# Kernel optimization log

Hardware: AMD Instinct MI355X
Metric: run time of the kernel (lower is better)

The kernel has to match this reference:

```python
import jax, jax.numpy as jnp
import numpy as np

K = 3          # deformable conv kernel size
PAD = 1        # (K-1)//2
G = 4          # deformable groups


def setup_inputs() -> dict:
    key = jax.random.key(0)
    k1, k2, k3, k4 = jax.random.split(key, 4)
    B, Cin, Cout, H, W = 8, 256, 256, 64, 64
    NA = 9  # num_anchors
    x = jax.random.normal(k1, (B, Cin, H, W), jnp.float32)
    shape = jax.random.normal(k2, (B, NA * 4, H, W), jnp.float32)
    # conv_offset: 1x1 conv, no bias -> weight (G*2*K*K, NA*4); std=0.1 per init_weights
    w_off = jax.random.normal(k3, (G * 2 * K * K, NA * 4), jnp.float32) * 0.1
    # conv_adaption (DeformConv, no bias): weight (Cout, Cin, K, K); std=0.01
    w_def = jax.random.normal(k4, (Cout, Cin, K, K), jnp.float32) * 0.01
    return {"x": x, "shape": shape, "w_off": w_off, "w_def": w_def}


def _deform_conv(x, offset, w):
    """DCNv1: x (B,Cin,H,W), offset (B,G*2*K*K,H,W) interleaved (dy,dx) per tap, w (Cout,Cin,K,K)."""
    B, Cin, H, W = x.shape
    Cout = w.shape[0]
    K2 = K * K
    Cg = Cin // G
    off = offset.reshape(B, G, K2, 2, H, W)  # [..., 0]=dy, [..., 1]=dx (mmcv layout)
    ky, kx = jnp.meshgrid(jnp.arange(K) - PAD, jnp.arange(K) - PAD, indexing='ij')
    ky = ky.reshape(K2).astype(x.dtype)
    kx = kx.reshape(K2).astype(x.dtype)
    hh = jnp.arange(H, dtype=x.dtype)
    ww = jnp.arange(W, dtype=x.dtype)
    # sampling positions: p = p0 + kernel_tap + learned_offset  -> (B,G,K2,H,W)
    py = off[:, :, :, 0] + ky[None, None, :, None, None] + hh[None, None, None, :, None]
    px = off[:, :, :, 1] + kx[None, None, :, None, None] + ww[None, None, None, None, :]

    y0f = jnp.floor(py)
    x0f = jnp.floor(px)
    wy1 = py - y0f
    wx1 = px - x0f
    y0 = y0f.astype(jnp.int32)
    x0 = x0f.astype(jnp.int32)

    img = x.reshape(B, G, Cg, H, W).transpose(0, 1, 3, 4, 2)  # (B,G,H,W,Cg) channels-last for gather
    b_idx = jnp.arange(B)[:, None, None, None, None]
    g_idx = jnp.arange(G)[None, :, None, None, None]

    def gather(yi, xi):
        valid = (yi >= 0) & (yi < H) & (xi >= 0) & (xi < W)
        yc = jnp.clip(yi, 0, H - 1)
        xc = jnp.clip(xi, 0, W - 1)
        v = img[b_idx, g_idx, yc, xc]  # (B,G,K2,H,W,Cg)
        return v * valid[..., None].astype(v.dtype)

    val = (gather(y0, x0) * ((1 - wy1) * (1 - wx1))[..., None]
           + gather(y0, x0 + 1) * ((1 - wy1) * wx1)[..., None]
           + gather(y0 + 1, x0) * (wy1 * (1 - wx1))[..., None]
           + gather(y0 + 1, x0 + 1) * (wy1 * wx1)[..., None])  # (B,G,K2,H,W,Cg)

    wr = w.reshape(Cout, G, Cg, K2)
    return jnp.einsum('bgkhwc,ogck->bohw', val, wr)


def reference(x, shape, w_off, w_def):
    # conv_offset: 1x1 conv, no bias, on detached shape prediction
    offset = jnp.einsum('bihw,oi->bohw', jax.lax.stop_gradient(shape), w_off)
    return jax.nn.relu(_deform_conv(x, offset, w_def))
```

## Files before the change

### kernel.cpp

```cpp
#include <hip/hip_runtime.h>
#include <hip/hip_bf16.h>


#define NPIX 32768
#define NGK  36
#define HW   4096
#define WSTRIDE 16384

typedef __attribute__((ext_vector_type(8))) short short8;
typedef __attribute__((ext_vector_type(4))) float f32x4;
typedef unsigned short u16;
typedef unsigned int u32;

__device__ __forceinline__ float bfu_lo(u32 u) {
    union { u32 u; float f; } cv; cv.u = u << 16; return cv.f;
}
__device__ __forceinline__ float bfu_hi(u32 u) {
    union { u32 u; float f; } cv; cv.u = u & 0xFFFF0000u; return cv.f;
}
__device__ __forceinline__ u16 f2bf(float f) {
    union { float f; u32 u; } cv;
    cv.f = f;
    u32 u = cv.u + 0x7FFFu + ((cv.u >> 16) & 1u);
    return (u16)(u >> 16);
}

__global__ __launch_bounds__(256) void kprep(const float* __restrict__ x,
                                             const float* __restrict__ shape,
                                             const float* __restrict__ w_off,
                                             const float* __restrict__ w_def,
                                             float2* __restrict__ pos,
                                             u16* __restrict__ xT,
                                             u16* __restrict__ wF) {
    __shared__ __align__(16) float smem[64 * 65];
    int tid = threadIdx.x;
    int blk = blockIdx.x;

    if (blk < 128) {
        float* wo = smem;
        for (int i = tid; i < 72 * 36; i += 256) wo[i] = w_off[i];
        __syncthreads();
        int pix = blk * 256 + tid;
        int b = pix >> 12, hw = pix & 4095;
        int h = hw >> 6, w = hw & 63;
        float s[36];
#pragma unroll
        for (int i = 0; i < 36; ++i) s[i] = shape[((b * 36 + i) << 12) + hw];
        for (int gk = 0; gk < 36; ++gk) {
            float oy = 0.f, ox = 0.f;
            const float* wy = &wo[(gk * 2 + 0) * 36];
            const float* wx = &wo[(gk * 2 + 1) * 36];
#pragma unroll
            for (int i = 0; i < 36; ++i) { oy += s[i] * wy[i]; ox += s[i] * wx[i]; }
            int k = gk % 9;
            pos[gk * NPIX + pix] = make_float2(oy + (float)(k / 3 - 1) + (float)h,
                                               ox + (float)(k % 3 - 1) + (float)w);
        }
    } else if (blk < 2176) {
        float (*tile)[65] = (float (*)[65])smem;
        int xb  = blk - 128;
        int bg  = xb >> 6;
        int hw0 = (xb & 63) << 6;
        int hwo = tid & 63;
#pragma unroll
        for (int i = 0; i < 16; ++i) {
            int c = (tid >> 6) + (i << 2);
            tile[c][hwo] = x[((bg << 6) + c) * HW + hw0 + hwo];
        }
        __syncthreads();
        int hw = tid >> 2;
        int cb4 = (tid & 3) << 4;
        short8 r0, r1;
#pragma unroll
        for (int j = 0; j < 8; ++j) {
            r0[j] = (short)f2bf(tile[cb4 + j][hw]);
            r1[j] = (short)f2bf(tile[cb4 + 8 + j][hw]);
        }
        u16* dst = xT + (((bg << 12) + hw0 + hw) << 6) + cb4;
        *(short8*)dst = r0;
        *(short8*)(dst + 8) = r1;
    } else {
        int idx = (blk - 2176) * 256 + tid;
        int c = idx & 63;
        int o = (idx >> 6) & 255;
        int gk = idx >> 14;
        int g = gk / 9, k = gk - g * 9;
        float v = w_def[((o << 8) + (g << 6) + c) * 9 + k];
        int wid = o >> 5, of = (o >> 4) & 1, olo = o & 15;
        int kc = c >> 5, cgran = (c >> 3) & 3, j = c & 7;
        int lane = (cgran << 4) | olo;
        wF[(gk << 14) + (wid << 11) + (of << 10) + (kc << 9) + (lane << 3) + j] = f2bf(v);
    }
}

struct Samp {
    short8 v00, v01, v10, v11;
    float w00, w01, w10, w11;
    int dst;
};

__device__ __forceinline__ Samp sample_issue_rec(uint2 ra, float4 rw,
                                                 const u16* __restrict__ slab,
                                                 int sp, int sck) {
    Samp s;
    int a00 = ra.x & 0xFFFF, a01 = ra.x >> 16;
    int a10 = ra.y & 0xFFFF, a11 = ra.y >> 16;
    const u16* base = slab + (sck << 3);
    s.v00 = *(const short8*)(base + (a00 << 6));
    s.v01 = *(const short8*)(base + (a01 << 6));
    s.v10 = *(const short8*)(base + (a10 << 6));
    s.v11 = *(const short8*)(base + (a11 << 6));
    s.w00 = rw.x; s.w01 = rw.y; s.w10 = rw.z; s.w11 = rw.w;
    s.dst = (sp << 6) + ((sck ^ (sp & 7)) << 3);
    return s;
}

__device__ __forceinline__ void sample_finish(const Samp& s, u16* __restrict__ sVb) {
    union { short8 s8; u32 u[4]; } A, Bc, C, D;
    A.s8 = s.v00; Bc.s8 = s.v01; C.s8 = s.v10; D.s8 = s.v11;
    union { u32 u[4]; short8 s8; } R;
#pragma unroll
    for (int j = 0; j < 4; ++j) {
        float lo0 = fmaf(s.w00, bfu_lo(A.u[j]), s.w01 * bfu_lo(Bc.u[j]));
        float lo1 = fmaf(s.w10, bfu_lo(C.u[j]), s.w11 * bfu_lo(D.u[j]));
        float hi0 = fmaf(s.w00, bfu_hi(A.u[j]), s.w01 * bfu_hi(Bc.u[j]));
        float hi1 = fmaf(s.w10, bfu_hi(C.u[j]), s.w11 * bfu_hi(D.u[j]));
        __hip_bfloat162 pk = __float22bfloat162_rn(make_float2(lo0 + lo1, hi0 + hi1));
        union { __hip_bfloat162 b; u32 u; } cv; cv.b = pk;
        R.u[j] = cv.u;
    }
    *(short8*)(sVb + s.dst) = R.s8;
}

__device__ __forceinline__ void mfma_phase(const short8 wcur[4], const u16* __restrict__ Vb,
                                           int lane, f32x4 acc[2][4]) {
    __builtin_amdgcn_s_setprio(1);
#pragma unroll
    for (int kc = 0; kc < 2; ++kc) {
        int cs = ((kc << 5) + ((lane >> 4) << 3)) ^ ((lane & 7) << 3);
        short8 bfr[4];
#pragma unroll
        for (int pf = 0; pf < 4; ++pf)
            bfr[pf] = *(const short8*)(Vb + (((pf << 4) + (lane & 15)) << 6) + cs);
#pragma unroll
        for (int of = 0; of < 2; ++of)
#pragma unroll
            for (int pf = 0; pf < 4; ++pf)
                acc[of][pf] = __builtin_amdgcn_mfma_f32_16x16x32_bf16(
                    wcur[of * 2 + kc], bfr[pf], acc[of][pf], 0, 0, 0);
    }
    __builtin_amdgcn_s_setprio(0);
}

__global__ __launch_bounds__(512, 4) void kmain(
    const u16* __restrict__ xT,
    const float2* __restrict__ pos,
    const u16* __restrict__ wF, float* __restrict__ out)
{
    __shared__ __align__(16) u16 sV[2][64 * 64];
    __shared__ __align__(16) uint2 sRA[NGK * 64];
    __shared__ __align__(16) float4 sRW[NGK * 64];

    int tid = threadIdx.x;
    int pixbase = blockIdx.x << 6;
    int b = pixbase >> 12;

    int sp = tid >> 3, sck = tid & 7;
    int lane = tid & 63, wid = tid >> 6;
    int o0 = wid << 5;

    const u16* slabB = xT + ((size_t)b << 20);
    const u16* wlbase = wF + (wid << 11) + (lane << 3);

    f32x4 acc[2][4];
#pragma unroll
    for (int i = 0; i < 2; ++i)
#pragma unroll
        for (int j = 0; j < 4; ++j)
            acc[i][j] = (f32x4){0.f, 0.f, 0.f, 0.f};

    short8 wC[4], wN[4];
    Samp s;

    for (int i = tid; i < NGK * 64; i += 512) {
        int gk = i >> 6, px = i & 63;
        float2 p = pos[gk * NPIX + pixbase + px];
        float py = p.x, pxx = p.y;
        float y0f = floorf(py), x0f = floorf(pxx);
        float fy = py - y0f, fx = pxx - x0f;
        int y0 = (int)y0f, x0 = (int)x0f;
        int y1 = y0 + 1, x1 = x0 + 1;
        float vy0 = (y0 >= 0 && y0 < 64) ? 1.f : 0.f;
        float vy1 = (y1 >= 0 && y1 < 64) ? 1.f : 0.f;
        float vx0 = (x0 >= 0 && x0 < 64) ? 1.f : 0.f;
        float vx1 = (x1 >= 0 && x1 < 64) ? 1.f : 0.f;
        float w00 = (1.f - fy) * (1.f - fx) * vy0 * vx0;
        float w01 = (1.f - fy) * fx * vy0 * vx1;
        float w10 = fy * (1.f - fx) * vy1 * vx0;
        float w11 = fy * fx * vy1 * vx1;
        int yc0 = min(max(y0, 0), 63), yc1 = min(max(y1, 0), 63);
        int xc0 = min(max(x0, 0), 63), xc1 = min(max(x1, 0), 63);
        u32 A = (u32)((yc0 << 6) | xc0) | ((u32)((yc0 << 6) | xc1) << 16);
        u32 Bp = (u32)((yc1 << 6) | xc0) | ((u32)((yc1 << 6) | xc1) << 16);
        sRA[i] = make_uint2(A, Bp);
        sRW[i] = make_float4(w00, w01, w10, w11);
    }

    wC[0] = *(const short8*)(wlbase);
    wC[1] = *(const short8*)(wlbase + 512);
    wC[2] = *(const short8*)(wlbase + 1024);
    wC[3] = *(const short8*)(wlbase + 1536);
    __syncthreads();

    {
        Samp s0 = sample_issue_rec(sRA[sp], sRW[sp], slabB, sp, sck);
        sample_finish(s0, sV[0]);
    }
    __syncthreads();

#define TAP_BODY(T, WCUR, WNXT)                                                  \
    {                                                                            \
        const int t_ = (T);                                                      \
        const u16* wn = wlbase + (t_ + 1) * WSTRIDE;                             \
        WNXT[0] = *(const short8*)(wn);                                          \
        WNXT[1] = *(const short8*)(wn + 512);                                    \
        WNXT[2] = *(const short8*)(wn + 1024);                                   \
        WNXT[3] = *(const short8*)(wn + 1536);                                   \
        s = sample_issue_rec(sRA[((t_ + 1) << 6) + sp], sRW[((t_ + 1) << 6) + sp], \
                             slabB + (((t_ + 1) / 9) << 18), sp, sck);           \
        __builtin_amdgcn_sched_barrier(0);                                       \
        mfma_phase(WCUR, sV[t_ & 1], lane, acc);                                 \
        sample_finish(s, sV[(t_ & 1) ^ 1]);                                      \
        __syncthreads();                                                         \
    }

    for (int t = 0; t < 34; t += 2) {
        TAP_BODY(t,     wC, wN)
        TAP_BODY(t + 1, wN, wC)
    }
#undef TAP_BODY

    {
        const u16* wn = wlbase + 35 * WSTRIDE;
        wN[0] = *(const short8*)(wn);
        wN[1] = *(const short8*)(wn + 512);
        wN[2] = *(const short8*)(wn + 1024);
        wN[3] = *(const short8*)(wn + 1536);
        s = sample_issue_rec(sRA[(35 << 6) + sp], sRW[(35 << 6) + sp],
                             slabB + (3 << 18), sp, sck);
        __builtin_amdgcn_sched_barrier(0);
        mfma_phase(wC, sV[0], lane, acc);
        sample_finish(s, sV[1]);
        __syncthreads();
    }
    mfma_phase(wN, sV[1], lane, acc);

    int hwb = pixbase & 4095;
    int obase = (b << 8) + o0 + ((lane >> 4) << 2);
#pragma unroll
    for (int of = 0; of < 2; ++of) {
#pragma unroll
        for (int pf = 0; pf < 4; ++pf) {
            float* op = out + ((obase + (of << 4)) << 12) + hwb + (pf << 4) + (lane & 15);
#pragma unroll
            for (int r = 0; r < 4; ++r)
                op[r << 12] = fmaxf(acc[of][pf][r], 0.f);
        }
    }
}

extern "C" void kernel_launch(void* const* d_in, const int* in_sizes, int n_in,
                              void* d_out, int out_size, void* d_ws, size_t ws_size,
                              hipStream_t stream) {
    const float* x     = (const float*)d_in[0];
    const float* shape = (const float*)d_in[1];
    const float* w_off = (const float*)d_in[2];
    const float* w_def = (const float*)d_in[3];
    float* out = (float*)d_out;

    float2* pos = (float2*)d_ws;
    u16*    wF  = (u16*)(pos + NGK * NPIX);
    u16*    xT  = wF + NGK * 256 * 64;

    kprep<<<4480, 256, 0, stream>>>(x, shape, w_off, w_def, pos, xT, wF);
    kmain<<<NPIX / 64, 512, 0, stream>>>(xT, pos, wF, out);
}
```

Before: 86.06 us.

## Process two taps per barrier with four LDS buffers and compact sample records

Restructures the main loop so each iteration samples two taps ahead into a four-slot LDS ring and runs two MFMA phases per barrier, halving the number of __syncthreads. The per-pixel bilinear weights are no longer stored as float4; validity flags are packed into the spare bits of the address record and only the fractional parts are stored, with the weights rebuilt at sample time. This cuts LDS record traffic and barrier count, at the cost of more registers held in flight (two sample sets plus two weight fragments) and some extra ALU work per sample, which may lower occupancy.

```diff
diff --git a/kernel.cpp b/kernel.cpp
--- a/kernel.cpp
+++ b/kernel.cpp
@@ -99,18 +99,25 @@
     int dst;
 };
 
-__device__ __forceinline__ Samp sample_issue_rec(uint2 ra, float4 rw,
+__device__ __forceinline__ Samp sample_issue_rec(uint2 ra, float2 fxy,
                                                  const u16* __restrict__ slab,
                                                  int sp, int sck) {
     Samp s;
-    int a00 = ra.x & 0xFFFF, a01 = ra.x >> 16;
-    int a10 = ra.y & 0xFFFF, a11 = ra.y >> 16;
+    u32 rx = ra.x, ry = ra.y;
+    int a00 = rx & 0xFFF, a01 = (rx >> 16) & 0xFFF;
+    int a10 = ry & 0xFFF, a11 = (ry >> 16) & 0xFFF;
     const u16* base = slab + (sck << 3);
     s.v00 = *(const short8*)(base + (a00 << 6));
     s.v01 = *(const short8*)(base + (a01 << 6));
     s.v10 = *(const short8*)(base + (a10 << 6));
     s.v11 = *(const short8*)(base + (a11 << 6));
-    s.w00 = rw.x; s.w01 = rw.y; s.w10 = rw.z; s.w11 = rw.w;
+    float fy = fxy.x, fx = fxy.y;
+    float wy0 = (rx & 0x1000u) ? (1.f - fy) : 0.f;
+    float wy1 = (rx & 0x2000u) ? fy : 0.f;
+    float wx0 = (rx & 0x4000u) ? (1.f - fx) : 0.f;
+    float wx1 = (rx & 0x8000u) ? fx : 0.f;
+    s.w00 = wy0 * wx0; s.w01 = wy0 * wx1;
+    s.w10 = wy1 * wx0; s.w11 = wy1 * wx1;
     s.dst = (sp << 6) + ((sck ^ (sp & 7)) << 3);
     return s;
 }
@@ -157,9 +164,9 @@
     const float2* __restrict__ pos,
     const u16* __restrict__ wF, float* __restrict__ out)
 {
-    __shared__ __align__(16) u16 sV[2][64 * 64];
+    __shared__ __align__(16) u16 sV[4][4096];
     __shared__ __align__(16) uint2 sRA[NGK * 64];
-    __shared__ __align__(16) float4 sRW[NGK * 64];
+    __shared__ __align__(16) float2 sFX[NGK * 64];
 
     int tid = threadIdx.x;
     int pixbase = blockIdx.x << 6;
@@ -179,81 +186,85 @@
         for (int j = 0; j < 4; ++j)
             acc[i][j] = (f32x4){0.f, 0.f, 0.f, 0.f};
 
-    short8 wC[4], wN[4];
-    Samp s;
+    short8 wE[4], wO[4];
 
     for (int i = tid; i < NGK * 64; i += 512) {
         int gk = i >> 6, px = i & 63;
         float2 p = pos[gk * NPIX + pixbase + px];
-        float py = p.x, pxx = p.y;
-        float y0f = floorf(py), x0f = floorf(pxx);
-        float fy = py - y0f, fx = pxx - x0f;
+        float y0f = floorf(p.x), x0f = floorf(p.y);
+        float fy = p.x - y0f, fx = p.y - x0f;
         int y0 = (int)y0f, x0 = (int)x0f;
         int y1 = y0 + 1, x1 = x0 + 1;
-        float vy0 = (y0 >= 0 && y0 < 64) ? 1.f : 0.f;
-        float vy1 = (y1 >= 0 && y1 < 64) ? 1.f : 0.f;
-        float vx0 = (x0 >= 0 && x0 < 64) ? 1.f : 0.f;
-        float vx1 = (x1 >= 0 && x1 < 64) ? 1.f : 0.f;
-        float w00 = (1.f - fy) * (1.f - fx) * vy0 * vx0;
-        float w01 = (1.f - fy) * fx * vy0 * vx1;
-        float w10 = fy * (1.f - fx) * vy1 * vx0;
-        float w11 = fy * fx * vy1 * vx1;
+        u32 flags = 0;
+        if (y0 >= 0 && y0 < 64) flags |= 0x1000u;
+        if (y1 >= 0 && y1 < 64) flags |= 0x2000u;
+        if (x0 >= 0 && x0 < 64) flags |= 0x4000u;
+        if (x1 >= 0 && x1 < 64) flags |= 0x8000u;
         int yc0 = min(max(y0, 0), 63), yc1 = min(max(y1, 0), 63);
         int xc0 = min(max(x0, 0), 63), xc1 = min(max(x1, 0), 63);
-        u32 A = (u32)((yc0 << 6) | xc0) | ((u32)((yc0 << 6) | xc1) << 16);
-        u32 Bp = (u32)((yc1 << 6) | xc0) | ((u32)((yc1 << 6) | xc1) << 16);
-        sRA[i] = make_uint2(A, Bp);
-        sRW[i] = make_float4(w00, w01, w10, w11);
-    }
-
-    wC[0] = *(const short8*)(wlbase);
-    wC[1] = *(const short8*)(wlbase + 512);
-    wC[2] = *(const short8*)(wlbase + 1024);
-    wC[3] = *(const short8*)(wlbase + 1536);
+        u32 a00 = (u32)((yc0 << 6) | xc0), a01 = (u32)((yc0 << 6) | xc1);
+        u32 a10 = (u32)((yc1 << 6) | xc0), a11 = (u32)((yc1 << 6) | xc1);
+        sRA[i] = make_uint2(a00 | flags | (a01 << 16), a10 | (a11 << 16));
+        sFX[i] = make_float2(fy, fx);
+    }
+
+    wE[0] = *(const short8*)(wlbase);
+    wE[1] = *(const short8*)(wlbase + 512);
+    wE[2] = *(const short8*)(wlbase + 1024);
+    wE[3] = *(const short8*)(wlbase + 1536);
     __syncthreads();
 
     {
-        Samp s0 = sample_issue_rec(sRA[sp], sRW[sp], slabB, sp, sck);
+        Samp s0 = sample_issue_rec(sRA[sp], sFX[sp], slabB, sp, sck);
         sample_finish(s0, sV[0]);
+        Samp s1 = sample_issue_rec(sRA[64 + sp], sFX[64 + sp], slabB, sp, sck);
+        sample_finish(s1, sV[1]);
     }
     __syncthreads();
 
-#define TAP_BODY(T, WCUR, WNXT)                                                  \
-    {                                                                            \
-        const int t_ = (T);                                                      \
-        const u16* wn = wlbase + (t_ + 1) * WSTRIDE;                             \
-        WNXT[0] = *(const short8*)(wn);                                          \
-        WNXT[1] = *(const short8*)(wn + 512);                                    \
-        WNXT[2] = *(const short8*)(wn + 1024);                                   \
-        WNXT[3] = *(const short8*)(wn + 1536);                                   \
-        s = sample_issue_rec(sRA[((t_ + 1) << 6) + sp], sRW[((t_ + 1) << 6) + sp], \
-                             slabB + (((t_ + 1) / 9) << 18), sp, sck);           \
-        __builtin_amdgcn_sched_barrier(0);                                       \
-        mfma_phase(WCUR, sV[t_ & 1], lane, acc);                                 \
-        sample_finish(s, sV[(t_ & 1) ^ 1]);                                      \
-        __syncthreads();                                                         \
-    }
-
-    for (int t = 0; t < 34; t += 2) {
-        TAP_BODY(t,     wC, wN)
-        TAP_BODY(t + 1, wN, wC)
-    }
-#undef TAP_BODY
+    for (int p = 0; p < 17; ++p) {
+        int t0 = p << 1;
+        int cur = (p & 1) << 1, nxt = cur ^ 2;
+
+        const u16* wop = wlbase + (t0 + 1) * WSTRIDE;
+        wO[0] = *(const short8*)(wop);
+        wO[1] = *(const short8*)(wop + 512);
+        wO[2] = *(const short8*)(wop + 1024);
+        wO[3] = *(const short8*)(wop + 1536);
+
+        int ta = t0 + 2, tb = t0 + 3;
+        Samp sA = sample_issue_rec(sRA[(ta << 6) + sp], sFX[(ta << 6) + sp],
+                                   slabB + ((ta / 9) << 18), sp, sck);
+        Samp sB = sample_issue_rec(sRA[(tb << 6) + sp], sFX[(tb << 6) + sp],
+                                   slabB + ((tb / 9) << 18), sp, sck);
+        __builtin_amdgcn_sched_barrier(0);
+
+        mfma_phase(wE, &sV[cur][0], lane, acc);
+
+        const u16* wep = wlbase + (t0 + 2) * WSTRIDE;
+        wE[0] = *(const short8*)(wep);
+        wE[1] = *(const short8*)(wep + 512);
+        wE[2] = *(const short8*)(wep + 1024);
+        wE[3] = *(const short8*)(wep + 1536);
+        __builtin_amdgcn_sched_barrier(0);
+
+        mfma_phase(wO, &sV[cur + 1][0], lane, acc);
+
+        sample_finish(sA, &sV[nxt][0]);
+        sample_finish(sB, &sV[nxt + 1][0]);
+        __syncthreads();
+    }
 
     {
-        const u16* wn = wlbase + 35 * WSTRIDE;
-        wN[0] = *(const short8*)(wn);
-        wN[1] = *(const short8*)(wn + 512);
-        wN[2] = *(const short8*)(wn + 1024);
-        wN[3] = *(const short8*)(wn + 1536);
-        s = sample_issue_rec(sRA[(35 << 6) + sp], sRW[(35 << 6) + sp],
-                             slabB + (3 << 18), sp, sck);
+        const u16* wop = wlbase + 35 * WSTRIDE;
+        wO[0] = *(const short8*)(wop);
+        wO[1] = *(const short8*)(wop + 512);
+        wO[2] = *(const short8*)(wop + 1024);
+        wO[3] = *(const short8*)(wop + 1536);
         __builtin_amdgcn_sched_barrier(0);
-        mfma_phase(wC, sV[0], lane, acc);
-        sample_finish(s, sV[1]);
-        __syncthreads();
-    }
-    mfma_phase(wN, sV[1], lane, acc);
+        mfma_phase(wE, &sV[2][0], lane, acc);
+        mfma_phase(wO, &sV[3][0], lane, acc);
+    }
 
     int hwb = pixbase & 4095;
     int obase = (b << 8) + o0 + ((lane >> 4) << 2);
```

Result: slower. 118.2 us (+37.4%).
